# Kernel tuning notes

Measured on AMD Instinct MI355X. Metric: run time of the kernel, lower is better.

## Reference

```python
import jax, jax.numpy as jnp
import numpy as np

GAMMA = 4  # channel groups (s)


def setup_inputs() -> dict:
    key = jax.random.key(0)
    k1, k2, k3, k4 = jax.random.split(key, 4)
    b, w, n, c = 16, 128, 256, 128  # batch, windows, win_size, channels
    x = jax.random.normal(k1, (b, w, n, c), dtype=jnp.float32)
    att_std = 0.01
    attention_centers = att_std * jax.random.normal(k2, (GAMMA, 1), dtype=jnp.float32)
    attention_spreads = 1.0 + att_std * jax.random.normal(k3, (GAMMA, 1), dtype=jnp.float32)
    token_proj_n_bias = 0.01 * jax.random.normal(k4, (1, n, 1), dtype=jnp.float32)
    return {"x": x, "attention_centers": attention_centers,
            "attention_spreads": attention_spreads,
            "token_proj_n_bias": token_proj_n_bias}


def _rel_indices(n):
    idx = jnp.arange(n, dtype=jnp.float32)
    d = idx[None, :] - idx[:, None]          # (n, n)
    return jnp.stack([d, d * d], axis=-1)     # (n, n, 2): [indx, indx^2]


def reference(x, attention_centers, attention_spreads, token_proj_n_bias):
    b, w, n, c = x.shape
    s = attention_centers.shape[0]
    v = c // s
    # pos_proj = -1/2 * [-2*delta*inv_cov, inv_cov]  -> (s, 2)
    pos_proj = -0.5 * jnp.concatenate(
        [-2.0 * attention_centers * attention_spreads, attention_spreads], axis=-1)
    rel = _rel_indices(n)                                   # (n, n, 2)
    pos_score = jnp.einsum('mnd,sd->mns', rel, pos_proj)    # (m, n, s)
    posmap = jax.nn.softmax(pos_score, axis=1)              # softmax over n
    xr = x.reshape(b, w, n, v, s)
    out = jnp.einsum('mns,bwnvs->bwmvs', posmap, xr)        # contract tokens n
    out = out + token_proj_n_bias[None, :, :, :, None]       # (1,1,n,1,1) broadcast
    return out.reshape(b, w, n, c)
```

## Files before the change

kernel.cpp:

```cpp
#include <hip/hip_runtime.h>
#include <hip/hip_bf16.h>


#define N_TOK 256
#define C_CH  128
#define NV    32
#define HW    8
#define TAPS  17
#define PMPAD 20
#define MCHUNK 64
#define ROWS  (MCHUNK + 2*HW)

__global__ void pm_build_kernel(const float* __restrict__ centers,
                                const float* __restrict__ spreads,
                                float* __restrict__ pmb) {
    const int m    = blockIdx.x;
    const int lane = threadIdx.x;
    const int n    = m + lane - HW;
    const bool valid = (lane < TAPS) && ((unsigned)n < N_TOK);
    const float dd = (float)(lane - HW);

    float e[4];
#pragma unroll
    for (int s = 0; s < 4; ++s) {
        const float ctr = centers[s];
        const float spr = spreads[s];
        const float sc = (ctr * spr) * dd - 0.5f * spr * dd * dd;
        e[s] = valid ? expf(sc) : 0.0f;
    }
#pragma unroll
    for (int s = 0; s < 4; ++s) {
        float v = e[s];
#pragma unroll
        for (int off = 32; off; off >>= 1) v += __shfl_xor(v, off, 64);
        const float denom = __shfl(v, 0, 64);
        e[s] = e[s] / denom;
    }
    if (lane < PMPAD) {
        reinterpret_cast<float4*>(pmb)[m * PMPAD + lane] =
            make_float4(e[0], e[1], e[2], e[3]);
    }
}

__global__ __launch_bounds__(512, 4)
void pm_apply_kernel(const float* __restrict__ x,
                     const float* __restrict__ pmb,
                     const float* __restrict__ bias,
                     float* __restrict__ out) {
    const int bw   = blockIdx.x;
    const int m0   = blockIdx.y * MCHUNK;
    const int row0 = m0 - HW;
    const int tid  = threadIdx.x;

    __shared__ float4 lds_x[ROWS * NV];
    __shared__ float4 lds_pm[MCHUNK * PMPAD];

    const float* xb = x + (size_t)bw * N_TOK * C_CH;

#pragma unroll
    for (int i = 0; i < (ROWS * NV) / 512; ++i) {
        const int idx = tid + i * 512;
        const int r = idx >> 5;
        const int v = idx & 31;
        int n = row0 + r;
        n = n < 0 ? 0 : (n > N_TOK - 1 ? N_TOK - 1 : n);
        lds_x[idx] = reinterpret_cast<const float4*>(xb + n * C_CH)[v];
    }
    {
        const float4* src = reinterpret_cast<const float4*>(pmb) + m0 * PMPAD;
        lds_pm[tid] = src[tid];
        lds_pm[tid + 512] = src[tid + 512];
        if (tid < 256) lds_pm[tid + 1024] = src[tid + 1024];
    }
    __syncthreads();

    const int v     = tid & 31;
    const int mslot = tid >> 5;
    const int mbase = m0 + mslot * 4;
    const int mloc  = mslot * 4;

    float4 acc[4];
#pragma unroll
    for (int mi = 0; mi < 4; ++mi) {
        const float bv = bias[mbase + mi];
        acc[mi] = make_float4(bv, bv, bv, bv);
    }

#pragma unroll
    for (int nr = 0; nr < 20; ++nr) {
        const float4 x4 = lds_x[(mloc + nr) * NV + v];
#pragma unroll
        for (int mi = 0; mi < 4; ++mi) {
            const int d = nr - mi;
            if (d >= 0 && d < TAPS) {
                const float4 p = lds_pm[(mloc + mi) * PMPAD + d];
                acc[mi].x += p.x * x4.x;
                acc[mi].y += p.y * x4.y;
                acc[mi].z += p.z * x4.z;
                acc[mi].w += p.w * x4.w;
            }
        }
    }

    float4* ob = reinterpret_cast<float4*>(out + (size_t)bw * N_TOK * C_CH);
#pragma unroll
    for (int mi = 0; mi < 4; ++mi) {
        ob[(mbase + mi) * NV + v] = acc[mi];
    }
}

extern "C" void kernel_launch(void* const* d_in, const int* in_sizes, int n_in,
                              void* d_out, int out_size, void* d_ws, size_t ws_size,
                              hipStream_t stream) {
    const float* x       = (const float*)d_in[0];
    const float* centers = (const float*)d_in[1];
    const float* spreads = (const float*)d_in[2];
    const float* bias    = (const float*)d_in[3];
    float* out = (float*)d_out;
    float* pmb = (float*)d_ws;

    pm_build_kernel<<<dim3(N_TOK), dim3(64), 0, stream>>>(centers, spreads, pmb);

    const int n_bw = 16 * 128;
    pm_apply_kernel<<<dim3(n_bw, N_TOK / MCHUNK), dim3(512), 0, stream>>>(
        x, pmb, bias, out);
}
```

Before: 114.3 us.

## Use direct global-to-LDS loads, halve block size with two channel groups per thread

Loads the x tile and the posmap taps straight into LDS with global_load_lds, so the data no longer passes through registers. Blocks shrink to 256 threads and each thread now computes two float4 channel groups, which reuses each posmap load across twice as many FMAs. The grid is transposed so neighbouring blocks cover neighbouring token chunks of the same window, which helps L2 reuse of the halo rows, and the posmap padding is cut to 18. Fewer threads per block and a launch-bounds hint of 2 may lower occupancy for this memory-bound kernel.

```diff
diff --git a/kernel.cpp b/kernel.cpp
--- a/kernel.cpp
+++ b/kernel.cpp
@@ -7,9 +7,14 @@
 #define NV    32
 #define HW    8
 #define TAPS  17
-#define PMPAD 20
+#define PMPAD 18
 #define MCHUNK 64
 #define ROWS  (MCHUNK + 2*HW)
+#define XFL4  (ROWS * NV)
+#define PMFL4 (MCHUNK * PMPAD)
+
+typedef const __attribute__((address_space(1))) void gvoid_t;
+typedef __attribute__((address_space(3))) void       lvoid_t;
 
 __global__ void pm_build_kernel(const float* __restrict__ centers,
                                 const float* __restrict__ spreads,
@@ -33,8 +38,7 @@
         float v = e[s];
 #pragma unroll
         for (int off = 32; off; off >>= 1) v += __shfl_xor(v, off, 64);
-        const float denom = __shfl(v, 0, 64);
-        e[s] = e[s] / denom;
+        e[s] = e[s] / __shfl(v, 0, 64);
     }
     if (lane < PMPAD) {
         reinterpret_cast<float4*>(pmb)[m * PMPAD + lane] =
@@ -42,70 +46,85 @@
     }
 }
 
-__global__ __launch_bounds__(512, 4)
+__global__ __launch_bounds__(256, 2)
 void pm_apply_kernel(const float* __restrict__ x,
                      const float* __restrict__ pmb,
                      const float* __restrict__ bias,
                      float* __restrict__ out) {
-    const int bw   = blockIdx.x;
-    const int m0   = blockIdx.y * MCHUNK;
+    const int m0   = blockIdx.x * MCHUNK;
+    const int bw   = blockIdx.y;
     const int row0 = m0 - HW;
     const int tid  = threadIdx.x;
 
-    __shared__ float4 lds_x[ROWS * NV];
-    __shared__ float4 lds_pm[MCHUNK * PMPAD];
+    __shared__ float4 lds_x[XFL4];
+    __shared__ float4 lds_pm[PMFL4];
 
-    const float* xb = x + (size_t)bw * N_TOK * C_CH;
+    const float* xb = x + (size_t)bw * (N_TOK * C_CH);
 
 #pragma unroll
-    for (int i = 0; i < (ROWS * NV) / 512; ++i) {
-        const int idx = tid + i * 512;
+    for (int i = 0; i < XFL4 / 256; ++i) {
+        const int idx = tid + i * 256;
         const int r = idx >> 5;
         const int v = idx & 31;
         int n = row0 + r;
         n = n < 0 ? 0 : (n > N_TOK - 1 ? N_TOK - 1 : n);
-        lds_x[idx] = reinterpret_cast<const float4*>(xb + n * C_CH)[v];
+        __builtin_amdgcn_global_load_lds((gvoid_t*)(xb + n * C_CH + v * 4),
+                                         (lvoid_t*)&lds_x[idx], 16, 0, 0);
     }
     {
         const float4* src = reinterpret_cast<const float4*>(pmb) + m0 * PMPAD;
-        lds_pm[tid] = src[tid];
-        lds_pm[tid + 512] = src[tid + 512];
-        if (tid < 256) lds_pm[tid + 1024] = src[tid + 1024];
+#pragma unroll
+        for (int i = 0; i < 5; ++i) {
+            const int idx = tid + i * 256;
+            if (idx < PMFL4) {
+                __builtin_amdgcn_global_load_lds((gvoid_t*)(src + idx),
+                                                 (lvoid_t*)&lds_pm[idx], 16, 0, 0);
+            }
+        }
     }
     __syncthreads();
 
-    const int v     = tid & 31;
-    const int mslot = tid >> 5;
-    const int mbase = m0 + mslot * 4;
+    const int vg    = tid & 15;
+    const int mslot = tid >> 4;
     const int mloc  = mslot * 4;
+    const int mbase = m0 + mloc;
+    const int c0 = vg, c1 = vg + 16;
 
-    float4 acc[4];
+    float4 acc[4][2];
 #pragma unroll
     for (int mi = 0; mi < 4; ++mi) {
         const float bv = bias[mbase + mi];
-        acc[mi] = make_float4(bv, bv, bv, bv);
+        acc[mi][0] = make_float4(bv, bv, bv, bv);
+        acc[mi][1] = acc[mi][0];
     }
 
 #pragma unroll
     for (int nr = 0; nr < 20; ++nr) {
-        const float4 x4 = lds_x[(mloc + nr) * NV + v];
+        const int rbase = (mloc + nr) * NV;
+        const float4 x0 = lds_x[rbase + c0];
+        const float4 x1 = lds_x[rbase + c1];
 #pragma unroll
         for (int mi = 0; mi < 4; ++mi) {
             const int d = nr - mi;
             if (d >= 0 && d < TAPS) {
                 const float4 p = lds_pm[(mloc + mi) * PMPAD + d];
-                acc[mi].x += p.x * x4.x;
-                acc[mi].y += p.y * x4.y;
-                acc[mi].z += p.z * x4.z;
-                acc[mi].w += p.w * x4.w;
+                acc[mi][0].x += p.x * x0.x;
+                acc[mi][0].y += p.y * x0.y;
+                acc[mi][0].z += p.z * x0.z;
+                acc[mi][0].w += p.w * x0.w;
+                acc[mi][1].x += p.x * x1.x;
+                acc[mi][1].y += p.y * x1.y;
+                acc[mi][1].z += p.z * x1.z;
+                acc[mi][1].w += p.w * x1.w;
             }
         }
     }
 
-    float4* ob = reinterpret_cast<float4*>(out + (size_t)bw * N_TOK * C_CH);
+    float4* ob = reinterpret_cast<float4*>(out + (size_t)bw * (N_TOK * C_CH));
 #pragma unroll
     for (int mi = 0; mi < 4; ++mi) {
-        ob[(mbase + mi) * NV + v] = acc[mi];
+        ob[(mbase + mi) * NV + c0] = acc[mi][0];
+        ob[(mbase + mi) * NV + c1] = acc[mi][1];
     }
 }
 
@@ -122,6 +141,6 @@
     pm_build_kernel<<<dim3(N_TOK), dim3(64), 0, stream>>>(centers, spreads, pmb);
 
     const int n_bw = 16 * 128;
-    pm_apply_kernel<<<dim3(n_bw, N_TOK / MCHUNK), dim3(512), 0, stream>>>(
+    pm_apply_kernel<<<dim3(N_TOK / MCHUNK, n_bw), dim3(256), 0, stream>>>(
         x, pmb, bias, out);
 }
```

New measurement: 110.0 us. 1.04x faster.

## Replace LDS-staged banded conv with register sliding window and scalar interior weights

Applied to the files above, without the earlier changes.

The apply kernel drops LDS staging and the block-wide sync. Each wave now streams a 64-row segment of one image through a register sliding window, prefetching the next 4 rows while the current group is computed. Interior rows share a single Toeplitz weight row that is held in scalar registers through readfirstlane. Edge rows near the sequence boundaries read their per-row weights from global memory. This removes redundant halo loads and LDS traffic, at the cost of higher register pressure and some serial latency within each wave.

```diff
diff --git a/kernel.cpp b/kernel.cpp
--- a/kernel.cpp
+++ b/kernel.cpp
@@ -7,9 +7,11 @@
 #define NV    32
 #define HW    8
 #define TAPS  17
-#define PMPAD 20
-#define MCHUNK 64
-#define ROWS  (MCHUNK + 2*HW)
+#define PMPAD 18
+#define SEG   64
+#define GS    4
+#define NG    (SEG / GS)
+#define WROWS (GS + 2 * HW)
 
 __global__ void pm_build_kernel(const float* __restrict__ centers,
                                 const float* __restrict__ spreads,
@@ -33,8 +35,7 @@
         float v = e[s];
 #pragma unroll
         for (int off = 32; off; off >>= 1) v += __shfl_xor(v, off, 64);
-        const float denom = __shfl(v, 0, 64);
-        e[s] = e[s] / denom;
+        e[s] = e[s] / __shfl(v, 0, 64);
     }
     if (lane < PMPAD) {
         reinterpret_cast<float4*>(pmb)[m * PMPAD + lane] =
@@ -42,70 +43,96 @@
     }
 }
 
-__global__ __launch_bounds__(512, 4)
+__global__ __launch_bounds__(256, 4)
 void pm_apply_kernel(const float* __restrict__ x,
                      const float* __restrict__ pmb,
                      const float* __restrict__ bias,
                      float* __restrict__ out) {
-    const int bw   = blockIdx.x;
-    const int m0   = blockIdx.y * MCHUNK;
-    const int row0 = m0 - HW;
     const int tid  = threadIdx.x;
+    const int wave = tid >> 6;
+    const int lane = tid & 63;
+    const int imgl = lane >> 5;
+    const int col  = lane & 31;
+    const int img  = (blockIdx.x << 1) | imgl;
+    const int m0   = wave * SEG;
 
-    __shared__ float4 lds_x[ROWS * NV];
-    __shared__ float4 lds_pm[MCHUNK * PMPAD];
+    const float4* xb = reinterpret_cast<const float4*>(x)
+                       + (size_t)img * (N_TOK * NV) + col;
+    float4*       ob = reinterpret_cast<float4*>(out)
+                       + (size_t)img * (N_TOK * NV) + col;
 
-    const float* xb = x + (size_t)bw * N_TOK * C_CH;
+    float wsc[TAPS * 4];
+    {
+        const float* wrow = pmb + 128 * (PMPAD * 4);
+#pragma unroll
+        for (int t = 0; t < TAPS * 4; ++t)
+            wsc[t] = __int_as_float(
+                __builtin_amdgcn_readfirstlane(__float_as_int(wrow[t])));
+    }
+
+    float4 R[WROWS];
+#pragma unroll
+    for (int i = 0; i < WROWS; ++i) {
+        int r = m0 - HW + i;
+        r = r < 0 ? 0 : r;
+        R[i] = xb[r * NV];
+    }
+    float4 Nx[GS];
+
+#pragma unroll 1
+    for (int g = 0; g < NG; ++g) {
+        const int mb = m0 + g * GS;
+
+        if (g < NG - 1) {
+#pragma unroll
+            for (int i = 0; i < GS; ++i) {
+                int r = mb + GS + HW + i;
+                r = r > N_TOK - 1 ? N_TOK - 1 : r;
+                Nx[i] = xb[r * NV];
+            }
+        }
+
+        const bool edge = (m0 == 0 && g < 2) || (m0 == 192 && g >= NG - 2);
+        if (!edge) {
+#pragma unroll
+            for (int j = 0; j < GS; ++j) {
+                const int m = mb + j;
+                const float bv = bias[m];
+                float ax = bv, ay = bv, az = bv, aw = bv;
+#pragma unroll
+                for (int t = 0; t < TAPS; ++t) {
+                    const float4 xv = R[j + t];
+                    ax += wsc[t * 4 + 0] * xv.x;
+                    ay += wsc[t * 4 + 1] * xv.y;
+                    az += wsc[t * 4 + 2] * xv.z;
+                    aw += wsc[t * 4 + 3] * xv.w;
+                }
+                ob[m * NV] = make_float4(ax, ay, az, aw);
+            }
+        } else {
+#pragma unroll
+            for (int j = 0; j < GS; ++j) {
+                const int m = mb + j;
+                const float bv = bias[m];
+                float ax = bv, ay = bv, az = bv, aw = bv;
+                const float4* pmrow = reinterpret_cast<const float4*>(pmb) + m * PMPAD;
+#pragma unroll
+                for (int t = 0; t < TAPS; ++t) {
+                    const float4 w  = pmrow[t];
+                    const float4 xv = R[j + t];
+                    ax += w.x * xv.x;
+                    ay += w.y * xv.y;
+                    az += w.z * xv.z;
+                    aw += w.w * xv.w;
+                }
+                ob[m * NV] = make_float4(ax, ay, az, aw);
+            }
+        }
 
 #pragma unroll
-    for (int i = 0; i < (ROWS * NV) / 512; ++i) {
-        const int idx = tid + i * 512;
-        const int r = idx >> 5;
-        const int v = idx & 31;
-        int n = row0 + r;
-        n = n < 0 ? 0 : (n > N_TOK - 1 ? N_TOK - 1 : n);
-        lds_x[idx] = reinterpret_cast<const float4*>(xb + n * C_CH)[v];
-    }
-    {
-        const float4* src = reinterpret_cast<const float4*>(pmb) + m0 * PMPAD;
-        lds_pm[tid] = src[tid];
-        lds_pm[tid + 512] = src[tid + 512];
-        if (tid < 256) lds_pm[tid + 1024] = src[tid + 1024];
-    }
-    __syncthreads();
-
-    const int v     = tid & 31;
-    const int mslot = tid >> 5;
-    const int mbase = m0 + mslot * 4;
-    const int mloc  = mslot * 4;
-
-    float4 acc[4];
+        for (int i = 0; i < WROWS - GS; ++i) R[i] = R[i + GS];
 #pragma unroll
-    for (int mi = 0; mi < 4; ++mi) {
-        const float bv = bias[mbase + mi];
-        acc[mi] = make_float4(bv, bv, bv, bv);
-    }
-
-#pragma unroll
-    for (int nr = 0; nr < 20; ++nr) {
-        const float4 x4 = lds_x[(mloc + nr) * NV + v];
-#pragma unroll
-        for (int mi = 0; mi < 4; ++mi) {
-            const int d = nr - mi;
-            if (d >= 0 && d < TAPS) {
-                const float4 p = lds_pm[(mloc + mi) * PMPAD + d];
-                acc[mi].x += p.x * x4.x;
-                acc[mi].y += p.y * x4.y;
-                acc[mi].z += p.z * x4.z;
-                acc[mi].w += p.w * x4.w;
-            }
-        }
-    }
-
-    float4* ob = reinterpret_cast<float4*>(out + (size_t)bw * N_TOK * C_CH);
-#pragma unroll
-    for (int mi = 0; mi < 4; ++mi) {
-        ob[(mbase + mi) * NV + v] = acc[mi];
+        for (int i = 0; i < GS; ++i) R[WROWS - GS + i] = Nx[i];
     }
 }
 
@@ -121,7 +148,7 @@
 
     pm_build_kernel<<<dim3(N_TOK), dim3(64), 0, stream>>>(centers, spreads, pmb);
 
-    const int n_bw = 16 * 128;
-    pm_apply_kernel<<<dim3(n_bw, N_TOK / MCHUNK), dim3(512), 0, stream>>>(
+    const int n_imgpair = (16 * 128) / 2;
+    pm_apply_kernel<<<dim3(n_imgpair), dim3(256), 0, stream>>>(
         x, pmb, bias, out);
 }
```

After: 134.2 us. 17.5% more time.
